# Kernel optimization log

Measured on AMD Instinct MI355X. Metric: run time of the kernel, lower is better.

The kernel has to match this reference:

```python
import jax, jax.numpy as jnp
import numpy as np

N_E = 1024      # nconcepts (codebook size)
E_DIM = 64      # cdim (codebook vector dim)
BETA = 0.25
LEGACY = True


def setup_inputs() -> dict:
    key = jax.random.key(0)
    k1, k2, k3 = jax.random.split(key, 3)
    z_ = jax.random.normal(k1, (32, 256, 32, 32), jnp.float32)
    # 1x1 conv dis_modulator: 256 -> 64 channels (stored as [out, in])
    conv_w = jax.random.normal(k2, (64, 256), jnp.float32) / np.sqrt(256.0)
    conv_b = jnp.zeros((64,), jnp.float32)
    # embedding.weight.data.uniform_(-1/n_e, 1/n_e)
    emb = jax.random.uniform(k3, (N_E, E_DIM), jnp.float32, -1.0 / N_E, 1.0 / N_E)
    return {"z_": z_, "conv_w": conv_w, "conv_b": conv_b, "emb": emb}


def _forward(z_, conv_w, conv_b, emb):
    sg = jax.lax.stop_gradient
    # dis_modulator: 1x1 conv == per-pixel linear map  (B,Cin,H,W)->(B,Cout,H,W)
    z = jnp.einsum('bchw,oc->bohw', z_, conv_w) + conv_b[None, :, None, None]
    B = z.shape[0]
    # torch .view(-1, e_dim): row-major flatten of (B,C,H,W) into chunks of e_dim
    zf = z.reshape(-1, E_DIM)  # [B*C*H*W/e_dim, e_dim]

    # contrastive term: mean pairwise cosine similarity of codebook rows
    d1 = emb @ emb.T                                  # [n_e, n_e]
    norms = jnp.linalg.norm(emb, axis=1)              # [n_e]
    cosine = d1 / (norms[:, None] * norms[None, :])
    contrastive = jnp.mean(cosine)

    # squared L2 distances: ||z||^2 + ||e||^2 - 2 z.e
    d = (jnp.sum(zf * zf, axis=1, keepdims=True)
         + jnp.sum(emb * emb, axis=1)[None, :]
         - 2.0 * (zf @ emb.T))                        # [N, n_e]
    idx = jnp.argmin(d, axis=1)                       # [N]
    z_q = emb[idx].reshape(z.shape)

    if LEGACY:
        loss = jnp.mean((sg(z_q) - z) ** 2) + BETA * jnp.mean((z_q - sg(z)) ** 2)
    else:
        loss = BETA * jnp.mean((sg(z_q) - z) ** 2) + jnp.mean((z_q - sg(z)) ** 2)
    # hessian_penalty(G, z_, G_z=z): G is an affine 1x1 conv, so the central
    # second difference G(z+x) - 2G(z) + G(z-x) is identically zero -> penalty = 0.
    loss = loss + contrastive

    # straight-through estimator
    z_q_st = z + sg(z_q - z)

    # replicate source exactly: flat zeros(B*n_e) scattered at codebook indices
    sampled = jnp.zeros((B * N_E,), z.dtype).at[idx].set(1.0).reshape(B, N_E)
    min_idx = idx.reshape(B, -1)
    return z_q_st, loss, sampled, min_idx


def reference(z_, conv_w, conv_b, emb):
    z_q, loss, sampled, min_idx = _forward(z_, conv_w, conv_b, emb)
    return z_q, loss, sampled, min_idx
```

## Files before the change

kernel.cpp:

```cpp
#include <hip/hip_runtime.h>

#define BATCH   32
#define CIN     256
#define COUT    64
#define HW      1024
#define NE      1024
#define ED      64
#define NROW    32768
#define ZTOT    2097152

#define OFF_LOSS 2097152
#define OFF_SAMP 2097153
#define OFF_IDX  2129921

#define CXSTR 132
#define CWSTR 68
#define ZROWS 68
#define EROWS 36

__global__ __launch_bounds__(256, 2) void k_pre(const float* __restrict__ x,
                                                const float* __restrict__ w,
                                                const float* __restrict__ bias,
                                                float* __restrict__ z,
                                                const float* __restrict__ emb,
                                                float* __restrict__ out_samp,
                                                float* __restrict__ enorm,
                                                float* __restrict__ cpart,
                                                unsigned int* __restrict__ counter) {
    __shared__ float SH[64 * CXSTR + 64 * CWSTR];
    int bx = blockIdx.x;
    int t  = threadIdx.x;

    if (bx < 128) {
        if (bx == 0 && t == 0) *counter = 0u;
        out_samp[bx * 256 + t] = 0.0f;
        return;
    }
    if (bx < 144) {
        float* invl = SH;
        float* S    = SH + 64;
        int b2 = bx - 128;
        int i0 = b2 * 64;
        if (t < 64) {
            const float* e = emb + (size_t)(i0 + t) * ED;
            float r8[8];
            #pragma unroll
            for (int s = 0; s < 8; s++) { float xx = e[s]; r8[s] = xx * xx; }
            #pragma unroll
            for (int m = 1; m < 8; m++) {
                #pragma unroll
                for (int s = 0; s < 8; s++) { float xx = e[8 * m + s]; r8[s] += xx * xx; }
            }
            float en = ((r8[0] + r8[1]) + (r8[2] + r8[3])) + ((r8[4] + r8[5]) + (r8[6] + r8[7]));
            invl[t] = 1.0f / sqrtf(en);
        }
        __syncthreads();
        int d = t & 63, q = t >> 6;
        float s = 0.0f;
        #pragma unroll
        for (int m = 0; m < 16; m++) {
            int il = q + 4 * m;
            s = fmaf(emb[(size_t)(i0 + il) * ED + d], invl[il], s);
        }
        S[t] = s;
        __syncthreads();
        if (t < 64)
            cpart[b2 * 64 + t] = (S[t] + S[t + 64]) + (S[t + 128] + S[t + 192]);
        return;
    }
    if (bx < 148) {
        int j = (bx - 144) * 256 + t;
        const float* e = emb + (size_t)j * ED;
        float r8[8];
        #pragma unroll
        for (int s = 0; s < 8; s++) { float xx = e[s]; r8[s] = xx * xx; }
        #pragma unroll
        for (int m = 1; m < 8; m++) {
            #pragma unroll
            for (int s = 0; s < 8; s++) { float xx = e[8 * m + s]; r8[s] += xx * xx; }
        }
        enorm[j] = ((r8[0] + r8[1]) + (r8[2] + r8[3])) + ((r8[4] + r8[5]) + (r8[6] + r8[7]));
        return;
    }

    float* Xs = SH;
    float* Ws = SH + 64 * CXSTR;
    int cbx = bx - 148;
    int b   = cbx >> 3;
    int p0  = (cbx & 7) * 128;
    int pg  = t & 15;
    int og  = t >> 4;
    float acc[8][4];
    #pragma unroll
    for (int i = 0; i < 8; i++)
        #pragma unroll
        for (int j = 0; j < 4; j++) acc[i][j] = 0.0f;

    for (int c0 = 0; c0 < CIN; c0 += 64) {
        __syncthreads();
        {
            int u = t & 31, cc = t >> 5;
            #pragma unroll
            for (int m = 0; m < 8; m++) {
                int c = cc + 8 * m;
                float4 v = *(const float4*)&x[(size_t)(b * CIN + c0 + c) * HW + p0 + 4 * u];
                *(float4*)&Xs[c * CXSTR + 4 * u] = v;
            }
            int u2 = t & 15, o2 = t >> 4;
            #pragma unroll
            for (int m = 0; m < 4; m++) {
                int o = o2 + 16 * m;
                float4 v = *(const float4*)&w[o * CIN + c0 + 4 * u2];
                Ws[(4 * u2 + 0) * CWSTR + o] = v.x;
                Ws[(4 * u2 + 1) * CWSTR + o] = v.y;
                Ws[(4 * u2 + 2) * CWSTR + o] = v.z;
                Ws[(4 * u2 + 3) * CWSTR + o] = v.w;
            }
        }
        __syncthreads();
        #pragma unroll 4
        for (int k = 0; k < 64; k++) {
            float4 xa4 = *(const float4*)&Xs[k * CXSTR + 4 * pg];
            float4 xb4 = *(const float4*)&Xs[k * CXSTR + 64 + 4 * pg];
            float4 wv4 = *(const float4*)&Ws[k * CWSTR + 4 * og];
            float xa[8] = {xa4.x, xa4.y, xa4.z, xa4.w, xb4.x, xb4.y, xb4.z, xb4.w};
            float wb[4] = {wv4.x, wv4.y, wv4.z, wv4.w};
            #pragma unroll
            for (int i = 0; i < 8; i++)
                #pragma unroll
                for (int j = 0; j < 4; j++)
                    acc[i][j] = fmaf(xa[i], wb[j], acc[i][j]);
        }
    }
    #pragma unroll
    for (int j = 0; j < 4; j++) {
        int o = 4 * og + j;
        float bv = bias[o];
        float4 lo, hi;
        lo.x = acc[0][j] + bv; lo.y = acc[1][j] + bv;
        lo.z = acc[2][j] + bv; lo.w = acc[3][j] + bv;
        hi.x = acc[4][j] + bv; hi.y = acc[5][j] + bv;
        hi.z = acc[6][j] + bv; hi.w = acc[7][j] + bv;
        *(float4*)&z[(size_t)(b * COUT + o) * HW + p0 + 4 * pg]      = lo;
        *(float4*)&z[(size_t)(b * COUT + o) * HW + p0 + 64 + 4 * pg] = hi;
    }
}

__global__ __launch_bounds__(256, 2) void k_dist(const float* __restrict__ z,
                                                 const float* __restrict__ emb,
                                                 const float* __restrict__ enorm,
                                                 const float* __restrict__ cpart,
                                                 float* __restrict__ out_idx,
                                                 float* __restrict__ out_samp,
                                                 float* __restrict__ out_zq,
                                                 float* __restrict__ ssep,
                                                 float* __restrict__ out_loss,
                                                 unsigned int* __restrict__ counter) {
    __shared__ float zs[64 * ZROWS];
    __shared__ float es[256 * EROWS];
    __shared__ float zn_s[64];
    __shared__ float en_s[256];
    __shared__ float warr[4];
    __shared__ int   lastflag;
    __shared__ float CS;
    float* redd_s = es;
    int*   redj_s = (int*)(es + 2048);
    int*   bj_s   = (int*)(es + 4096);
    int t = threadIdx.x;
    int row0 = blockIdx.x * 64;
    int rg = t >> 5;
    int cg = t & 31;

    {
        int k4 = t & 15, rr = t >> 4;
        #pragma unroll
        for (int m = 0; m < 4; m++) {
            int r = rr + 16 * m;
            float4 v = *(const float4*)&z[(size_t)(row0 + r) * ED + 4 * k4];
            *(float4*)&zs[r * ZROWS + 4 * k4] = v;
        }
    }
    __syncthreads();
    if (t < 64) {
        const float* zr = &zs[t * ZROWS];
        float r8[8];
        #pragma unroll
        for (int s = 0; s < 8; s++) { float xx = zr[s]; r8[s] = xx * xx; }
        #pragma unroll
        for (int m = 1; m < 8; m++) {
            #pragma unroll
            for (int s = 0; s < 8; s++) { float xx = zr[8 * m + s]; r8[s] += xx * xx; }
        }
        zn_s[t] = ((r8[0] + r8[1]) + (r8[2] + r8[3])) + ((r8[4] + r8[5]) + (r8[6] + r8[7]));
    }

    float bestd[8];
    int   bestj[8];
    #pragma unroll
    for (int i = 0; i < 8; i++) { bestd[i] = __builtin_huge_valf(); bestj[i] = 0; }

    for (int ch = 0; ch < 4; ch++) {
        int c0 = ch * 256;
        float acc[8][8];
        #pragma unroll
        for (int i = 0; i < 8; i++)
            #pragma unroll
            for (int j = 0; j < 8; j++) acc[i][j] = 0.0f;

        for (int kh = 0; kh < 2; kh++) {
            __syncthreads();
            {
                int k4 = t & 7, cc = t >> 3;
                #pragma unroll
                for (int m = 0; m < 8; m++) {
                    int c = cc + 32 * m;
                    float4 v = *(const float4*)&emb[(size_t)(c0 + c) * ED + kh * 32 + 4 * k4];
                    *(float4*)&es[c * EROWS + 4 * k4] = v;
                }
                if (kh == 0 && t < 64) {
                    float4 ev = *(const float4*)&enorm[c0 + 4 * t];
                    *(float4*)&en_s[4 * t] = ev;
                }
            }
            __syncthreads();

            int kb = kh * 32;
            #pragma unroll 2
            for (int ks = 0; ks < 8; ks++) {
                float4 za[8], eb[8];
                #pragma unroll
                for (int i = 0; i < 8; i++)
                    za[i] = *(const float4*)&zs[(rg + 8 * i) * ZROWS + kb + 4 * ks];
                #pragma unroll
                for (int j = 0; j < 8; j++)
                    eb[j] = *(const float4*)&es[(cg + 32 * j) * EROWS + 4 * ks];
                #pragma unroll
                for (int i = 0; i < 8; i++)
                    #pragma unroll
                    for (int j = 0; j < 8; j++) {
                        acc[i][j] = fmaf(za[i].x, eb[j].x, acc[i][j]);
                        acc[i][j] = fmaf(za[i].y, eb[j].y, acc[i][j]);
                        acc[i][j] = fmaf(za[i].z, eb[j].z, acc[i][j]);
                        acc[i][j] = fmaf(za[i].w, eb[j].w, acc[i][j]);
                    }
            }
        }

        #pragma unroll
        for (int i = 0; i < 8; i++) {
            float zn = zn_s[rg + 8 * i];
            #pragma unroll
            for (int j = 0; j < 8; j++) {
                int cl = cg + 32 * j;
                float A = zn + en_s[cl];
                float D = A - 2.0f * acc[i][j];
                if (D < bestd[i]) { bestd[i] = D; bestj[i] = c0 + cl; }
            }
        }
    }

    __syncthreads();
    #pragma unroll
    for (int i = 0; i < 8; i++) {
        int rl = rg + 8 * i;
        redd_s[cg * 64 + rl] = bestd[i];
        redj_s[cg * 64 + rl] = bestj[i];
    }
    __syncthreads();
    if (t < 64) {
        float bd = __builtin_huge_valf();
        int   bj = 0x7fffffff;
        #pragma unroll
        for (int c = 0; c < 32; c++) {
            float dd = redd_s[c * 64 + t];
            int   jj = redj_s[c * 64 + t];
            if (dd < bd || (dd == bd && jj < bj)) { bd = dd; bj = jj; }
        }
        int rowg = row0 + t;
        bj_s[t]       = bj;
        out_idx[rowg] = (float)bj;
        atomicExch(&out_samp[bj], 1.0f);
    }
    __syncthreads();

    {
        int r  = t & 63;
        int kq = t >> 6;
        int bj = bj_s[r];
        const float* er = emb + (size_t)bj * ED + kq * 16;
        const float* zr = &zs[r * ZROWS + kq * 16];
        float sq = 0.0f;
        #pragma unroll
        for (int m = 0; m < 4; m++) {
            float4 ev = *(const float4*)&er[4 * m];
            float4 zv = *(const float4*)&zr[4 * m];
            float d0 = ev.x - zv.x, d1 = ev.y - zv.y, d2 = ev.z - zv.z, d3 = ev.w - zv.w;
            float4 o4;
            o4.x = zv.x + d0; o4.y = zv.y + d1; o4.z = zv.z + d2; o4.w = zv.w + d3;
            *(float4*)&out_zq[(size_t)(row0 + r) * ED + kq * 16 + 4 * m] = o4;
            sq += d0 * d0; sq += d1 * d1; sq += d2 * d2; sq += d3 * d3;
        }
        #pragma unroll
        for (int off = 32; off > 0; off >>= 1) sq += __shfl_down(sq, off, 64);
        if ((t & 63) == 0) warr[t >> 6] = sq;
    }
    __syncthreads();

    if (t == 0) {
        ssep[blockIdx.x] = (warr[0] + warr[1]) + (warr[2] + warr[3]);
        __threadfence();
        unsigned int old = atomicAdd(counter, 1u);
        lastflag = (old == 511u) ? 1 : 0;
    }
    __syncthreads();
    if (lastflag) {
        __threadfence();
        double* SD = (double*)es;
        const volatile float* sv = (const volatile float*)ssep;
        SD[t] = (double)sv[t] + (double)sv[t + 256];
        __syncthreads();
        #pragma unroll
        for (int off = 128; off > 0; off >>= 1) {
            if (t < off) SD[t] += SD[t + off];
            __syncthreads();
        }
        if (t < 64) {
            float v = 0.0f;
            #pragma unroll
            for (int m = 0; m < 16; m++) v += cpart[m * 64 + t];
            float sq = v * v;
            #pragma unroll
            for (int off = 32; off > 0; off >>= 1) sq += __shfl_down(sq, off, 64);
            if (t == 0) CS = sq / (1024.0f * 1024.0f);
        }
        __syncthreads();
        if (t == 0) {
            float m = (float)(SD[0] / (double)ZTOT);
            float loss = m + 0.25f * m;
            out_loss[0] = loss + CS;
        }
    }
}

extern "C" void kernel_launch(void* const* d_in, const int* in_sizes, int n_in,
                              void* d_out, int out_size, void* d_ws, size_t ws_size,
                              hipStream_t stream) {
    (void)in_sizes; (void)n_in; (void)out_size; (void)ws_size;
    const float* z_     = (const float*)d_in[0];
    const float* conv_w = (const float*)d_in[1];
    const float* conv_b = (const float*)d_in[2];
    const float* emb    = (const float*)d_in[3];

    float* out      = (float*)d_out;
    float* out_zq   = out;
    float* out_loss = out + OFF_LOSS;
    float* out_samp = out + OFF_SAMP;
    float* out_idx  = out + OFF_IDX;

    char*  ws       = (char*)d_ws;
    float* wz       = (float*)ws;
    float* enorm    = (float*)(ws + 8388608);
    float* cpart    = (float*)(ws + 8392704);
    float* ssep     = (float*)(ws + 8396800);
    unsigned int* counter = (unsigned int*)(ws + 8398848);

    k_pre  <<<404, 256, 0, stream>>>(z_, conv_w, conv_b, wz, emb, out_samp, enorm, cpart, counter);
    k_dist <<<512, 256, 0, stream>>>(wz, emb, enorm, cpart, out_idx, out_samp, out_zq, ssep, out_loss, counter);
}
```

Before: 185.3 us.

## Transpose shared-memory tiles in distance GEMM and shrink conv tiles

The distance kernel now stores z and codebook tiles k-major (transposed) in shared memory, so each thread reads contiguous float4 runs of 8 rows and 8 codes per k step instead of strided row-major float4 loads. The thread mapping changes to give each thread contiguous rows and columns. The conv kernel uses smaller 64-pixel tiles with a 4x4 register block and higher occupancy, launching 512 GEMM blocks first in the grid. The transposed global loads are scalar and strided, which may cost uncoalesced traffic, and the row-norm is now read from global memory.

```diff
diff --git a/kernel.cpp b/kernel.cpp
--- a/kernel.cpp
+++ b/kernel.cpp
@@ -13,12 +13,11 @@
 #define OFF_SAMP 2097153
 #define OFF_IDX  2129921
 
-#define CXSTR 132
-#define CWSTR 68
-#define ZROWS 68
-#define EROWS 36
-
-__global__ __launch_bounds__(256, 2) void k_pre(const float* __restrict__ x,
+#define CXSTR 68
+#define ZKSTR 68
+#define EKSTR 260
+
+__global__ __launch_bounds__(256, 4) void k_pre(const float* __restrict__ x,
                                                 const float* __restrict__ w,
                                                 const float* __restrict__ bias,
                                                 float* __restrict__ z,
@@ -27,19 +26,79 @@
                                                 float* __restrict__ enorm,
                                                 float* __restrict__ cpart,
                                                 unsigned int* __restrict__ counter) {
-    __shared__ float SH[64 * CXSTR + 64 * CWSTR];
+    __shared__ float SH[64 * CXSTR * 2];
     int bx = blockIdx.x;
     int t  = threadIdx.x;
 
-    if (bx < 128) {
-        if (bx == 0 && t == 0) *counter = 0u;
-        out_samp[bx * 256 + t] = 0.0f;
+    if (bx < 512) {
+        float* Xs = SH;
+        float* Ws = SH + 64 * CXSTR;
+        int b  = bx >> 4;
+        int p0 = (bx & 15) * 64;
+        int pg = t & 15;
+        int og = t >> 4;
+        float acc[4][4];
+        #pragma unroll
+        for (int i = 0; i < 4; i++)
+            #pragma unroll
+            for (int j = 0; j < 4; j++) acc[i][j] = 0.0f;
+
+        for (int c0 = 0; c0 < CIN; c0 += 64) {
+            __syncthreads();
+            {
+                int u = t & 15, cg2 = t >> 4;
+                #pragma unroll
+                for (int m = 0; m < 4; m++) {
+                    int c = cg2 + 16 * m;
+                    float4 v = *(const float4*)&x[(size_t)(b * CIN + c0 + c) * HW + p0 + 4 * u];
+                    *(float4*)&Xs[c * CXSTR + 4 * u] = v;
+                }
+                #pragma unroll
+                for (int m = 0; m < 4; m++) {
+                    int o = cg2 + 16 * m;
+                    float4 v = *(const float4*)&w[o * CIN + c0 + 4 * u];
+                    Ws[(4 * u + 0) * CXSTR + o] = v.x;
+                    Ws[(4 * u + 1) * CXSTR + o] = v.y;
+                    Ws[(4 * u + 2) * CXSTR + o] = v.z;
+                    Ws[(4 * u + 3) * CXSTR + o] = v.w;
+                }
+            }
+            __syncthreads();
+            #pragma unroll 8
+            for (int k = 0; k < 64; k++) {
+                float4 xv = *(const float4*)&Xs[k * CXSTR + 4 * pg];
+                float4 wv = *(const float4*)&Ws[k * CXSTR + 4 * og];
+                float xa[4] = {xv.x, xv.y, xv.z, xv.w};
+                float wb[4] = {wv.x, wv.y, wv.z, wv.w};
+                #pragma unroll
+                for (int i = 0; i < 4; i++)
+                    #pragma unroll
+                    for (int j = 0; j < 4; j++)
+                        acc[i][j] = fmaf(xa[i], wb[j], acc[i][j]);
+            }
+        }
+        #pragma unroll
+        for (int j = 0; j < 4; j++) {
+            int o = 4 * og + j;
+            float bv = bias[o];
+            float4 out;
+            out.x = acc[0][j] + bv;
+            out.y = acc[1][j] + bv;
+            out.z = acc[2][j] + bv;
+            out.w = acc[3][j] + bv;
+            *(float4*)&z[(size_t)(b * COUT + o) * HW + p0 + 4 * pg] = out;
+        }
         return;
     }
-    if (bx < 144) {
+    if (bx < 640) {
+        if (bx == 512 && t == 0) *counter = 0u;
+        out_samp[(bx - 512) * 256 + t] = 0.0f;
+        return;
+    }
+    if (bx < 656) {
         float* invl = SH;
         float* S    = SH + 64;
-        int b2 = bx - 128;
+        int b2 = bx - 640;
         int i0 = b2 * 64;
         if (t < 64) {
             const float* e = emb + (size_t)(i0 + t) * ED;
@@ -68,8 +127,8 @@
             cpart[b2 * 64 + t] = (S[t] + S[t + 64]) + (S[t + 128] + S[t + 192]);
         return;
     }
-    if (bx < 148) {
-        int j = (bx - 144) * 256 + t;
+    {
+        int j = (bx - 656) * 256 + t;
         const float* e = emb + (size_t)j * ED;
         float r8[8];
         #pragma unroll
@@ -80,69 +139,6 @@
             for (int s = 0; s < 8; s++) { float xx = e[8 * m + s]; r8[s] += xx * xx; }
         }
         enorm[j] = ((r8[0] + r8[1]) + (r8[2] + r8[3])) + ((r8[4] + r8[5]) + (r8[6] + r8[7]));
-        return;
-    }
-
-    float* Xs = SH;
-    float* Ws = SH + 64 * CXSTR;
-    int cbx = bx - 148;
-    int b   = cbx >> 3;
-    int p0  = (cbx & 7) * 128;
-    int pg  = t & 15;
-    int og  = t >> 4;
-    float acc[8][4];
-    #pragma unroll
-    for (int i = 0; i < 8; i++)
-        #pragma unroll
-        for (int j = 0; j < 4; j++) acc[i][j] = 0.0f;
-
-    for (int c0 = 0; c0 < CIN; c0 += 64) {
-        __syncthreads();
-        {
-            int u = t & 31, cc = t >> 5;
-            #pragma unroll
-            for (int m = 0; m < 8; m++) {
-                int c = cc + 8 * m;
-                float4 v = *(const float4*)&x[(size_t)(b * CIN + c0 + c) * HW + p0 + 4 * u];
-                *(float4*)&Xs[c * CXSTR + 4 * u] = v;
-            }
-            int u2 = t & 15, o2 = t >> 4;
-            #pragma unroll
-            for (int m = 0; m < 4; m++) {
-                int o = o2 + 16 * m;
-                float4 v = *(const float4*)&w[o * CIN + c0 + 4 * u2];
-                Ws[(4 * u2 + 0) * CWSTR + o] = v.x;
-                Ws[(4 * u2 + 1) * CWSTR + o] = v.y;
-                Ws[(4 * u2 + 2) * CWSTR + o] = v.z;
-                Ws[(4 * u2 + 3) * CWSTR + o] = v.w;
-            }
-        }
-        __syncthreads();
-        #pragma unroll 4
-        for (int k = 0; k < 64; k++) {
-            float4 xa4 = *(const float4*)&Xs[k * CXSTR + 4 * pg];
-            float4 xb4 = *(const float4*)&Xs[k * CXSTR + 64 + 4 * pg];
-            float4 wv4 = *(const float4*)&Ws[k * CWSTR + 4 * og];
-            float xa[8] = {xa4.x, xa4.y, xa4.z, xa4.w, xb4.x, xb4.y, xb4.z, xb4.w};
-            float wb[4] = {wv4.x, wv4.y, wv4.z, wv4.w};
-            #pragma unroll
-            for (int i = 0; i < 8; i++)
-                #pragma unroll
-                for (int j = 0; j < 4; j++)
-                    acc[i][j] = fmaf(xa[i], wb[j], acc[i][j]);
-        }
-    }
-    #pragma unroll
-    for (int j = 0; j < 4; j++) {
-        int o = 4 * og + j;
-        float bv = bias[o];
-        float4 lo, hi;
-        lo.x = acc[0][j] + bv; lo.y = acc[1][j] + bv;
-        lo.z = acc[2][j] + bv; lo.w = acc[3][j] + bv;
-        hi.x = acc[4][j] + bv; hi.y = acc[5][j] + bv;
-        hi.z = acc[6][j] + bv; hi.w = acc[7][j] + bv;
-        *(float4*)&z[(size_t)(b * COUT + o) * HW + p0 + 4 * pg]      = lo;
-        *(float4*)&z[(size_t)(b * COUT + o) * HW + p0 + 64 + 4 * pg] = hi;
     }
 }
 
@@ -156,8 +152,8 @@
                                                  float* __restrict__ ssep,
                                                  float* __restrict__ out_loss,
                                                  unsigned int* __restrict__ counter) {
-    __shared__ float zs[64 * ZROWS];
-    __shared__ float es[256 * EROWS];
+    __shared__ float zs[64 * ZKSTR];
+    __shared__ float es[32 * EKSTR];
     __shared__ float zn_s[64];
     __shared__ float en_s[256];
     __shared__ float warr[4];
@@ -168,21 +164,24 @@
     int*   bj_s   = (int*)(es + 4096);
     int t = threadIdx.x;
     int row0 = blockIdx.x * 64;
-    int rg = t >> 5;
-    int cg = t & 31;
+    int rg = t & 7;
+    int cg = t >> 3;
 
     {
-        int k4 = t & 15, rr = t >> 4;
+        int k = t & 63, wv = t >> 6;
         #pragma unroll
         for (int m = 0; m < 4; m++) {
-            int r = rr + 16 * m;
-            float4 v = *(const float4*)&z[(size_t)(row0 + r) * ED + 4 * k4];
-            *(float4*)&zs[r * ZROWS + 4 * k4] = v;
-        }
-    }
-    __syncthreads();
+            int v = wv + 4 * m;
+            float4 val;
+            val.x = z[(size_t)(row0 + 4 * v + 0) * ED + k];
+            val.y = z[(size_t)(row0 + 4 * v + 1) * ED + k];
+            val.z = z[(size_t)(row0 + 4 * v + 2) * ED + k];
+            val.w = z[(size_t)(row0 + 4 * v + 3) * ED + k];
+            *(float4*)&zs[k * ZKSTR + 4 * v] = val;
+        }
+    }
     if (t < 64) {
-        const float* zr = &zs[t * ZROWS];
+        const float* zr = z + (size_t)(row0 + t) * ED;
         float r8[8];
         #pragma unroll
         for (int s = 0; s < 8; s++) { float xx = zr[s]; r8[s] = xx * xx; }
@@ -208,14 +207,19 @@
             for (int j = 0; j < 8; j++) acc[i][j] = 0.0f;
 
         for (int kh = 0; kh < 2; kh++) {
+            int kb = kh * 32;
             __syncthreads();
             {
-                int k4 = t & 7, cc = t >> 3;
+                int k = t & 31, wv = t >> 5;
                 #pragma unroll
                 for (int m = 0; m < 8; m++) {
-                    int c = cc + 32 * m;
-                    float4 v = *(const float4*)&emb[(size_t)(c0 + c) * ED + kh * 32 + 4 * k4];
-                    *(float4*)&es[c * EROWS + 4 * k4] = v;
+                    int v = wv + 8 * m;
+                    float4 val;
+                    val.x = emb[(size_t)(c0 + 4 * v + 0) * ED + kb + k];
+                    val.y = emb[(size_t)(c0 + 4 * v + 1) * ED + kb + k];
+                    val.z = emb[(size_t)(c0 + 4 * v + 2) * ED + kb + k];
+                    val.w = emb[(size_t)(c0 + 4 * v + 3) * ED + kb + k];
+                    *(float4*)&es[k * EKSTR + 4 * v] = val;
                 }
                 if (kh == 0 && t < 64) {
                     float4 ev = *(const float4*)&enorm[c0 + 4 * t];
@@ -224,34 +228,28 @@
             }
             __syncthreads();
 
-            int kb = kh * 32;
-            #pragma unroll 2
-            for (int ks = 0; ks < 8; ks++) {
-                float4 za[8], eb[8];
-                #pragma unroll
-                for (int i = 0; i < 8; i++)
-                    za[i] = *(const float4*)&zs[(rg + 8 * i) * ZROWS + kb + 4 * ks];
-                #pragma unroll
-                for (int j = 0; j < 8; j++)
-                    eb[j] = *(const float4*)&es[(cg + 32 * j) * EROWS + 4 * ks];
+            #pragma unroll 4
+            for (int kk = 0; kk < 32; kk++) {
+                float4 za0 = *(const float4*)&zs[(kb + kk) * ZKSTR + 8 * rg];
+                float4 za1 = *(const float4*)&zs[(kb + kk) * ZKSTR + 8 * rg + 4];
+                float4 eb0 = *(const float4*)&es[kk * EKSTR + 8 * cg];
+                float4 eb1 = *(const float4*)&es[kk * EKSTR + 8 * cg + 4];
+                float xa[8] = {za0.x, za0.y, za0.z, za0.w, za1.x, za1.y, za1.z, za1.w};
+                float eb[8] = {eb0.x, eb0.y, eb0.z, eb0.w, eb1.x, eb1.y, eb1.z, eb1.w};
                 #pragma unroll
                 for (int i = 0; i < 8; i++)
                     #pragma unroll
-                    for (int j = 0; j < 8; j++) {
-                        acc[i][j] = fmaf(za[i].x, eb[j].x, acc[i][j]);
-                        acc[i][j] = fmaf(za[i].y, eb[j].y, acc[i][j]);
-                        acc[i][j] = fmaf(za[i].z, eb[j].z, acc[i][j]);
-                        acc[i][j] = fmaf(za[i].w, eb[j].w, acc[i][j]);
-                    }
+                    for (int j = 0; j < 8; j++)
+                        acc[i][j] = fmaf(xa[i], eb[j], acc[i][j]);
             }
         }
 
         #pragma unroll
         for (int i = 0; i < 8; i++) {
-            float zn = zn_s[rg + 8 * i];
+            float zn = zn_s[8 * rg + i];
             #pragma unroll
             for (int j = 0; j < 8; j++) {
-                int cl = cg + 32 * j;
+                int cl = 8 * cg + j;
                 float A = zn + en_s[cl];
                 float D = A - 2.0f * acc[i][j];
                 if (D < bestd[i]) { bestd[i] = D; bestj[i] = c0 + cl; }
@@ -262,7 +260,7 @@
     __syncthreads();
     #pragma unroll
     for (int i = 0; i < 8; i++) {
-        int rl = rg + 8 * i;
+        int rl = 8 * rg + i;
         redd_s[cg * 64 + rl] = bestd[i];
         redj_s[cg * 64 + rl] = bestj[i];
     }
@@ -288,16 +286,19 @@
         int kq = t >> 6;
         int bj = bj_s[r];
         const float* er = emb + (size_t)bj * ED + kq * 16;
-        const float* zr = &zs[r * ZROWS + kq * 16];
         float sq = 0.0f;
         #pragma unroll
         for (int m = 0; m < 4; m++) {
             float4 ev = *(const float4*)&er[4 * m];
-            float4 zv = *(const float4*)&zr[4 * m];
-            float d0 = ev.x - zv.x, d1 = ev.y - zv.y, d2 = ev.z - zv.z, d3 = ev.w - zv.w;
+            int kk = kq * 16 + 4 * m;
+            float zv0 = zs[(kk + 0) * ZKSTR + r];
+            float zv1 = zs[(kk + 1) * ZKSTR + r];
+            float zv2 = zs[(kk + 2) * ZKSTR + r];
+            float zv3 = zs[(kk + 3) * ZKSTR + r];
+            float d0 = ev.x - zv0, d1 = ev.y - zv1, d2 = ev.z - zv2, d3 = ev.w - zv3;
             float4 o4;
-            o4.x = zv.x + d0; o4.y = zv.y + d1; o4.z = zv.z + d2; o4.w = zv.w + d3;
-            *(float4*)&out_zq[(size_t)(row0 + r) * ED + kq * 16 + 4 * m] = o4;
+            o4.x = zv0 + d0; o4.y = zv1 + d1; o4.z = zv2 + d2; o4.w = zv3 + d3;
+            *(float4*)&out_zq[(size_t)(row0 + r) * ED + kk] = o4;
             sq += d0 * d0; sq += d1 * d1; sq += d2 * d2; sq += d3 * d3;
         }
         #pragma unroll
@@ -364,6 +365,6 @@
     float* ssep     = (float*)(ws + 8396800);
     unsigned int* counter = (unsigned int*)(ws + 8398848);
 
-    k_pre  <<<404, 256, 0, stream>>>(z_, conv_w, conv_b, wz, emb, out_samp, enorm, cpart, counter);
+    k_pre  <<<660, 256, 0, stream>>>(z_, conv_w, conv_b, wz, emb, out_samp, enorm, cpart, counter);
     k_dist <<<512, 256, 0, stream>>>(wz, emb, enorm, cpart, out_idx, out_samp, out_zq, ssep, out_loss, counter);
 }
```

New measurement: 169.3 us. 8.7% less time.
